# Performance work log

Hardware: AMD Instinct MI355X
Metric: run time of the kernel (lower is better)

Reference implementation:

```python
import jax, jax.numpy as jnp
import numpy as np

BATCH = 16384
NUM_FIELDS = 20
NUM_FEATURES = 100000
LATENT_DIM = 64


def setup_inputs() -> dict:
    key = jax.random.key(0)
    k_x, k_e = jax.random.split(key)
    x = jax.random.randint(k_x, (BATCH, NUM_FIELDS), 0, NUM_FEATURES, dtype=jnp.int32)
    field_indices = jnp.arange(NUM_FIELDS, dtype=jnp.int32)
    # one embedding table per field, stacked: [F, num_features, D]
    emb = jax.random.normal(k_e, (NUM_FIELDS, NUM_FEATURES, LATENT_DIM), dtype=jnp.float32)
    return {"x": x, "field_indices": field_indices, "emb": emb}


def reference(x, field_indices, emb):
    # linear part: sum of raw integer indices over fields (as in the torch code)
    linear = jnp.sum(x, axis=1).astype(emb.dtype)  # [B]
    F = emb.shape[0]
    # gather v_i = emb[i][x[:, i]] for all fields at once -> [B, F, D]
    V = emb[jnp.arange(F)[None, :], x]
    # sum_{i<j} <v_i, v_j> = 0.5 * (||sum_i v_i||^2 - sum_i ||v_i||^2)
    s = jnp.sum(V, axis=1)                           # [B, D]
    interaction = 0.5 * (jnp.sum(s * s, axis=-1) - jnp.sum(V * V, axis=(1, 2)))  # [B]
    return linear + interaction
```

## Files before the change

kernel.cpp:

```cpp
#include <hip/hip_runtime.h>


constexpr int BATCH = 16384;
constexpr int NUM_FIELDS = 20;
constexpr int NUM_FEATURES = 100000;
constexpr int LATENT = 64;

__global__ __launch_bounds__(256)
void ffm_kernel(const int* __restrict__ x,
                const float* __restrict__ emb,
                float* __restrict__ out) {
    const int wave_in_block = threadIdx.x >> 6;
    const int lane          = threadIdx.x & 63;
    const int row           = blockIdx.x * 4 + wave_in_block;
    if (row >= BATCH) return;

    const int* xr = x + row * NUM_FIELDS;

    float s    = 0.0f;
    float sq   = 0.0f;
    float xsum = 0.0f;

#pragma unroll
    for (int f = 0; f < NUM_FIELDS; ++f) {
        const int idx = xr[f];
        xsum += (float)idx;
        const int off = (f * NUM_FEATURES + idx) * LATENT + lane;
        const float v = emb[off];
        s  += v;
        sq += v * v;
    }

    float t = 0.5f * (s * s - sq);

#pragma unroll
    for (int off = 32; off > 0; off >>= 1)
        t += __shfl_down(t, off, 64);

    if (lane == 0)
        out[row] = xsum + t;
}

extern "C" void kernel_launch(void* const* d_in, const int* in_sizes, int n_in,
                              void* d_out, int out_size, void* d_ws, size_t ws_size,
                              hipStream_t stream) {
    const int*   x   = (const int*)d_in[0];
    const float* emb = (const float*)d_in[2];
    float*       out = (float*)d_out;

    const int rows_per_block = 4;
    const int grid = (BATCH + rows_per_block - 1) / rows_per_block;
    ffm_kernel<<<grid, 256, 0, stream>>>(x, emb, out);
}
```

Baseline: 559.7 us.

## Vectorize embedding gathers to float4 with field-parallel lanes per wave

Each wave now splits its 64 lanes into 4 groups of 16. Each group loads a different field's 64-float embedding row with float4 loads, so 5 iterations replace 20 scalar gather steps. The per-group partial sums are combined with xor shuffles across the groups, and the interaction is computed with rescaled coefficients so that every lane holds the dot product redundantly. The aim is fewer, wider memory instructions and more loads in flight per wave. The cost is extra cross-lane shuffles, and the row bounds check is removed on the assumption that BATCH divides evenly.

```diff
diff --git a/kernel.cpp b/kernel.cpp
--- a/kernel.cpp
+++ b/kernel.cpp
@@ -1,44 +1,58 @@
 #include <hip/hip_runtime.h>
 
 
-constexpr int BATCH = 16384;
-constexpr int NUM_FIELDS = 20;
+constexpr int BATCH        = 16384;
+constexpr int NUM_FIELDS   = 20;
 constexpr int NUM_FEATURES = 100000;
-constexpr int LATENT = 64;
+constexpr int LATENT       = 64;
 
 __global__ __launch_bounds__(256)
 void ffm_kernel(const int* __restrict__ x,
                 const float* __restrict__ emb,
                 float* __restrict__ out) {
-    const int wave_in_block = threadIdx.x >> 6;
-    const int lane          = threadIdx.x & 63;
-    const int row           = blockIdx.x * 4 + wave_in_block;
-    if (row >= BATCH) return;
+    const int wave = threadIdx.x >> 6;
+    const int lane = threadIdx.x & 63;
+    const int row  = blockIdx.x * 4 + wave;
+
+    const int q = lane >> 4;
+    const int r = lane & 15;
 
     const int* xr = x + row * NUM_FIELDS;
 
-    float s    = 0.0f;
-    float sq   = 0.0f;
-    float xsum = 0.0f;
+    float4 s  = make_float4(0.f, 0.f, 0.f, 0.f);
+    float  sq = 0.f;
+    float  xs = 0.f;
 
 #pragma unroll
-    for (int f = 0; f < NUM_FIELDS; ++f) {
+    for (int i = 0; i < 5; ++i) {
+        const int f   = 4 * i + q;
         const int idx = xr[f];
-        xsum += (float)idx;
-        const int off = (f * NUM_FEATURES + idx) * LATENT + lane;
-        const float v = emb[off];
-        s  += v;
-        sq += v * v;
+        xs += (float)idx;
+        const int off = (f * NUM_FEATURES + idx) * LATENT + 4 * r;
+        const float4 v = *reinterpret_cast<const float4*>(emb + off);
+        s.x += v.x; s.y += v.y; s.z += v.z; s.w += v.w;
+        sq  += v.x * v.x + v.y * v.y + v.z * v.z + v.w * v.w;
     }
 
-    float t = 0.5f * (s * s - sq);
+#pragma unroll
+    for (int m = 16; m < 64; m <<= 1) {
+        s.x += __shfl_xor(s.x, m, 64);
+        s.y += __shfl_xor(s.y, m, 64);
+        s.z += __shfl_xor(s.z, m, 64);
+        s.w += __shfl_xor(s.w, m, 64);
+    }
+
+    const float dot = s.x * s.x + s.y * s.y + s.z * s.z + s.w * s.w;
+    float u = 0.125f * dot - 0.5f * sq;
+
+    if (r == 0) u += xs;
 
 #pragma unroll
-    for (int off = 32; off > 0; off >>= 1)
-        t += __shfl_down(t, off, 64);
+    for (int m = 32; m > 0; m >>= 1)
+        u += __shfl_xor(u, m, 64);
 
     if (lane == 0)
-        out[row] = xsum + t;
+        out[row] = u;
 }
 
 extern "C" void kernel_launch(void* const* d_in, const int* in_sizes, int n_in,
@@ -49,6 +63,6 @@
     float*       out = (float*)d_out;
 
     const int rows_per_block = 4;
-    const int grid = (BATCH + rows_per_block - 1) / rows_per_block;
+    const int grid = BATCH / rows_per_block;
     ffm_kernel<<<grid, 256, 0, stream>>>(x, emb, out);
 }
```

Result: no change. 560.5 us (+0.1%).
